# Performance work log

Measured on AMD Instinct MI355X. Metric: run time of the kernel, lower is better.

The kernel has to match this reference:

```python
import jax, jax.numpy as jnp
import numpy as np

D_MODEL = 1024
NUM_HEADS = 16
D_HEAD = D_MODEL // NUM_HEADS


def setup_inputs() -> dict:
    key = jax.random.key(0)
    kx, kq, kk, kv, ko = jax.random.split(key, 5)
    b, seq = 4, 2048
    x = jax.random.normal(kx, (b, seq, D_MODEL), dtype=jnp.float32)
    # Original uses ones for q/k/v and randn for output; use small random weights
    # for a numerically meaningful baseline of the same math.
    Wq = jax.random.normal(kq, (D_MODEL, D_MODEL), dtype=jnp.float32) * 0.02
    Wk = jax.random.normal(kk, (D_MODEL, D_MODEL), dtype=jnp.float32) * 0.02
    Wv = jax.random.normal(kv, (D_MODEL, D_MODEL), dtype=jnp.float32) * 0.02
    Wo = jax.random.normal(ko, (D_MODEL, D_MODEL), dtype=jnp.float32) * 0.02
    return {"x": x, "Wq": Wq, "Wk": Wk, "Wv": Wv, "Wo": Wo}


def reference(x, Wq, Wk, Wv, Wo):
    b, seq, d = x.shape
    h, dh = NUM_HEADS, D_HEAD

    def split_heads(t):  # [b, s, d] -> [b, h, s, dh]
        return t.reshape(b, seq, h, dh).transpose(0, 2, 1, 3)

    q = split_heads(x @ Wq.T)
    k = split_heads(x @ Wk.T)
    v = split_heads(x @ Wv.T)

    scores = jnp.einsum('bhqd,bhkd->bhqk', q, k) / jnp.sqrt(jnp.float32(dh))
    causal = jnp.tril(jnp.ones((seq, seq), dtype=bool))
    scores = jnp.where(causal, scores, -jnp.inf)
    attn = jax.nn.softmax(scores, axis=-1)
    out = jnp.einsum('bhqk,bhkd->bhqd', attn, v)  # [b, h, s, dh]
    out = out.transpose(0, 2, 1, 3).reshape(b, seq, d)
    return out @ Wo.T
```

## Files before the change

### kernel.cpp

```cpp
#include <hip/hip_runtime.h>
#include <stdint.h>

typedef unsigned short u16;
typedef __attribute__((ext_vector_type(8))) __bf16 bf16x8;
typedef __attribute__((ext_vector_type(4))) float f32x4;

#define AS1 __attribute__((address_space(1)))
#define AS3 __attribute__((address_space(3)))
#define LOG2E 1.4426950408889634f

__device__ __forceinline__ u16 f2bf(float f) {
    union { __bf16 h; u16 u; } cv;
    cv.h = (__bf16)f;
    return cv.u;
}

__device__ __forceinline__ float vmax4(f32x4 x) {
    return fmaxf(fmaxf(x[0], x[1]), fmaxf(x[2], x[3]));
}
__device__ __forceinline__ float vsum4(f32x4 x) {
    return (x[0] + x[1]) + (x[2] + x[3]);
}

__global__ __launch_bounds__(256) void cvt_kernel(
    const float* __restrict__ src, u16* __restrict__ dst, int n8)
{
    int i = blockIdx.x * 256 + threadIdx.x;
    if (i >= n8) return;
    const float4* s = (const float4*)src;
    float4 f0 = s[(size_t)i * 2], f1 = s[(size_t)i * 2 + 1];
    ushort4 a, b;
    a.x = f2bf(f0.x); a.y = f2bf(f0.y); a.z = f2bf(f0.z); a.w = f2bf(f0.w);
    b.x = f2bf(f1.x); b.y = f2bf(f1.y); b.z = f2bf(f1.z); b.w = f2bf(f1.w);
    ((ushort4*)dst)[(size_t)i * 2]     = a;
    ((ushort4*)dst)[(size_t)i * 2 + 1] = b;
}

__global__ __launch_bounds__(256) void cvt3_kernel(
    const float* __restrict__ wq, const float* __restrict__ wk,
    const float* __restrict__ wv, u16* __restrict__ dst)
{
    int i = blockIdx.x * 256 + threadIdx.x;
    int seg = i >> 17;
    const float* s = (seg == 0) ? wq : (seg == 1) ? wk : wv;
    float sc = (seg == 0) ? 0.125f : 1.0f;
    int j = i & 131071;
    const float4* sp = (const float4*)s;
    float4 f0 = sp[(size_t)j * 2], f1 = sp[(size_t)j * 2 + 1];
    ushort4 a, b;
    a.x = f2bf(f0.x * sc); a.y = f2bf(f0.y * sc); a.z = f2bf(f0.z * sc); a.w = f2bf(f0.w * sc);
    b.x = f2bf(f1.x * sc); b.y = f2bf(f1.y * sc); b.z = f2bf(f1.z * sc); b.w = f2bf(f1.w * sc);
    ((ushort4*)dst)[(size_t)i * 2]     = a;
    ((ushort4*)dst)[(size_t)i * 2 + 1] = b;
}

template <bool F32OUT>
__device__ __forceinline__ void gemm_tile_body(
    const u16* __restrict__ A, const u16* __restrict__ B, void* __restrict__ Cp,
    int K, int ldc, int mb, int nb, int cb, u16* As, u16* Bs)
{
    const int t  = threadIdx.x;
    const int l  = t & 63, w = t >> 6;
    const int wm = w >> 1, wn = w & 1;
    const int lr = l & 15, lg = l >> 4;

    f32x4 acc[4][4];
#pragma unroll
    for (int i = 0; i < 4; ++i)
#pragma unroll
        for (int j = 0; j < 4; ++j) acc[i][j] = f32x4{0.f, 0.f, 0.f, 0.f};

    for (int k0 = 0; k0 < K; k0 += 32) {
        __syncthreads();
#pragma unroll
        for (int i = 0; i < 2; ++i) {
            int chunk = i * 256 + t;
            int row   = chunk >> 2;
            int c8    = (chunk & 3) << 3;
            const u16* ga = A + (size_t)(mb + row) * K + k0 + c8;
            const u16* gb = B + (size_t)(nb + row) * K + k0 + c8;
            u16* la = As + (i * 256 + w * 64) * 8;
            u16* lb = Bs + (i * 256 + w * 64) * 8;
            __builtin_amdgcn_global_load_lds((AS1 unsigned int*)ga, (AS3 unsigned int*)la, 16, 0, 0);
            __builtin_amdgcn_global_load_lds((AS1 unsigned int*)gb, (AS3 unsigned int*)lb, 16, 0, 0);
        }
        __syncthreads();
        bf16x8 af[4], bfr[4];
#pragma unroll
        for (int mi = 0; mi < 4; ++mi)
            af[mi] = *(const bf16x8*)(As + (wm * 64 + mi * 16 + lr) * 32 + lg * 8);
#pragma unroll
        for (int ni = 0; ni < 4; ++ni)
            bfr[ni] = *(const bf16x8*)(Bs + (wn * 64 + ni * 16 + lr) * 32 + lg * 8);
#pragma unroll
        for (int mi = 0; mi < 4; ++mi)
#pragma unroll
            for (int ni = 0; ni < 4; ++ni)
                acc[mi][ni] = __builtin_amdgcn_mfma_f32_16x16x32_bf16(af[mi], bfr[ni], acc[mi][ni], 0, 0, 0);
    }
#pragma unroll
    for (int mi = 0; mi < 4; ++mi)
#pragma unroll
        for (int ni = 0; ni < 4; ++ni) {
            int col = cb + wn * 64 + ni * 16 + lr;
#pragma unroll
            for (int v = 0; v < 4; ++v) {
                int row = mb + wm * 64 + mi * 16 + lg * 4 + v;
                if (F32OUT)
                    ((float*)Cp)[(size_t)row * ldc + col] = acc[mi][ni][v];
                else
                    ((u16*)Cp)[(size_t)row * ldc + col] = f2bf(acc[mi][ni][v]);
            }
        }
}

__global__ __launch_bounds__(256, 2) void gemm_qkv_kernel(
    const u16* __restrict__ X, const u16* __restrict__ W3,
    u16* __restrict__ QKV)
{
    __shared__ __attribute__((aligned(16))) u16 As[128 * 32];
    __shared__ __attribute__((aligned(16))) u16 Bs[128 * 32];
    int bid = (int)blockIdx.x + (int)gridDim.x * (int)blockIdx.y;
    int wg  = (bid & 7) * 192 + (bid >> 3);
    int mx  = wg / 24;
    int my  = wg % 24;
    int wsel = my >> 3;
    const u16* B = W3 + (size_t)wsel * 1024 * 1024;
    int nb = (my & 7) * 128;
    gemm_tile_body<false>(X, B, QKV, 1024, 3072, mx * 128, nb, wsel * 1024 + nb, As, Bs);
}

__global__ __launch_bounds__(256, 2) void gemm_out_kernel(
    const u16* __restrict__ A, const u16* __restrict__ B, float* __restrict__ C)
{
    __shared__ __attribute__((aligned(16))) u16 As[128 * 32];
    __shared__ __attribute__((aligned(16))) u16 Bs[128 * 32];
    int bid = (int)blockIdx.x + (int)gridDim.x * (int)blockIdx.y;
    int wg  = (bid & 7) * 64 + (bid >> 3);
    int mx  = wg >> 3;
    int my  = wg & 7;
    gemm_tile_body<true>(A, B, C, 1024, 1024, mx * 128, my * 128, my * 128, As, Bs);
}

#define SEQ  2048
#define PSTR 72
#define NQT  16

__device__ __forceinline__ void attn_qtile(
    const u16* __restrict__ Qg, const u16* __restrict__ Kg, const u16* __restrict__ Vg,
    u16* __restrict__ outp, int b, int h, int qt,
    u16* QP, u16* Ks, u16* Vt)
{
    const int t  = threadIdx.x;
    const int l  = t & 63, w = t >> 6;
    const int lr = l & 15, lg = l >> 4;
    const int q0 = qt * 128;
    const int sr = t >> 3;
    const int sc = (t & 7) << 3;
    const int vswz = sc;

    __syncthreads();
#pragma unroll
    for (int i = 0; i < 4; ++i) {
        int r = sr + i * 32;
        *(uint4*)(QP + r * PSTR + sc) = *(const uint4*)(Qg + (size_t)(q0 + r) * 3072 + sc);
    }
    __syncthreads();
    bf16x8 qf[2][2];
#pragma unroll
    for (int mi = 0; mi < 2; ++mi)
#pragma unroll
        for (int ks = 0; ks < 2; ++ks)
            qf[mi][ks] = *(const bf16x8*)(QP + (w * 32 + mi * 16 + lr) * PSTR + ks * 32 + lg * 8);

    uint4 kpf[2], vpf[2];
#pragma unroll
    for (int i = 0; i < 2; ++i) {
        int r = sr + i * 32;
        kpf[i] = *(const uint4*)(Kg + (size_t)r * 3072 + sc);
        vpf[i] = *(const uint4*)(Vg + (size_t)r * 3072 + sc);
    }

    f32x4 o[4][2];
#pragma unroll
    for (int nd = 0; nd < 4; ++nd)
#pragma unroll
        for (int mi = 0; mi < 2; ++mi) o[nd][mi] = f32x4{0.f, 0.f, 0.f, 0.f};
    float mrow[2]  = { -__builtin_inff(), -__builtin_inff() };
    float mrowL[2] = { -__builtin_inff(), -__builtin_inff() };
    float lrow[2]  = { 0.f, 0.f };

    const int nkt = 2 * qt + 2;
    for (int kt = 0; kt < nkt; ++kt) {
        const int k0 = kt * 64;
        __syncthreads();
#pragma unroll
        for (int i = 0; i < 2; ++i) {
            int r = sr + i * 32;
            *(uint4*)(Ks + r * PSTR + sc) = kpf[i];
            int rs = r ^ vswz;
            union { uint4 q; u16 u[8]; } uv; uv.q = vpf[i];
#pragma unroll
            for (int j = 0; j < 8; ++j)
                Vt[(sc + j) * PSTR + rs] = uv.u[j];
        }
        if (kt + 1 < nkt) {
            const int k0n = k0 + 64;
#pragma unroll
            for (int i = 0; i < 2; ++i) {
                int r = sr + i * 32;
                kpf[i] = *(const uint4*)(Kg + (size_t)(k0n + r) * 3072 + sc);
                vpf[i] = *(const uint4*)(Vg + (size_t)(k0n + r) * 3072 + sc);
            }
        }
        __syncthreads();

        f32x4 s[4][2];
#pragma unroll
        for (int ni = 0; ni < 4; ++ni)
#pragma unroll
            for (int mi = 0; mi < 2; ++mi) s[ni][mi] = f32x4{0.f, 0.f, 0.f, 0.f};
        __builtin_amdgcn_s_setprio(1);
#pragma unroll
        for (int ks = 0; ks < 2; ++ks) {
            bf16x8 kb[4];
#pragma unroll
            for (int ni = 0; ni < 4; ++ni)
                kb[ni] = *(const bf16x8*)(Ks + (ni * 16 + lr) * PSTR + ks * 32 + lg * 8);
#pragma unroll
            for (int ni = 0; ni < 4; ++ni)
#pragma unroll
                for (int mi = 0; mi < 2; ++mi)
                    s[ni][mi] = __builtin_amdgcn_mfma_f32_16x16x32_bf16(kb[ni], qf[mi][ks], s[ni][mi], 0, 0, 0);
        }
        __builtin_amdgcn_s_setprio(0);

#pragma unroll
        for (int mi = 0; mi < 2; ++mi) {
            if ((k0 + 63) > (q0 + w * 32 + mi * 16)) {
                int qpos = q0 + w * 32 + mi * 16 + lr;
#pragma unroll
                for (int ni = 0; ni < 4; ++ni) {
                    int kb0 = k0 + ni * 16 + lg * 4;
#pragma unroll
                    for (int v = 0; v < 4; ++v)
                        if (kb0 + v > qpos) s[ni][mi][v] = -__builtin_inff();
                }
            }
        }

        float rmax[2];
        bool grew = false;
#pragma unroll
        for (int mi = 0; mi < 2; ++mi) {
            float r = fmaxf(fmaxf(vmax4(s[0][mi]), vmax4(s[1][mi])),
                            fmaxf(vmax4(s[2][mi]), vmax4(s[3][mi])));
            r = fmaxf(r, __shfl_xor(r, 16));
            r = fmaxf(r, __shfl_xor(r, 32));
            rmax[mi] = r;
            grew |= (r > mrow[mi]);
        }
        if (__ballot(grew)) {
#pragma unroll
            for (int mi = 0; mi < 2; ++mi) {
                float mn  = fmaxf(mrow[mi], rmax[mi]);
                float mnL = mn * LOG2E;
                float al  = __builtin_amdgcn_exp2f(mrowL[mi] - mnL);
                mrow[mi]  = mn;
                mrowL[mi] = mnL;
                lrow[mi] *= al;
#pragma unroll
                for (int nd = 0; nd < 4; ++nd)
#pragma unroll
                    for (int v = 0; v < 4; ++v) o[nd][mi][v] *= al;
            }
        }
#pragma unroll
        for (int mi = 0; mi < 2; ++mi) {
            float nmL = -mrowL[mi];
#pragma unroll
            for (int ni = 0; ni < 4; ++ni)
#pragma unroll
                for (int v = 0; v < 4; ++v)
                    s[ni][mi][v] = __builtin_amdgcn_exp2f(
                        __builtin_fmaf(s[ni][mi][v], LOG2E, nmL));
            float sum = (vsum4(s[0][mi]) + vsum4(s[1][mi]))
                      + (vsum4(s[2][mi]) + vsum4(s[3][mi]));
            sum += __shfl_xor(sum, 16);
            sum += __shfl_xor(sum, 32);
            lrow[mi] += sum;
            int prow = (w * 32 + mi * 16 + lr) * PSTR + lg * 4;
#pragma unroll
            for (int ni = 0; ni < 4; ++ni) {
                ushort4 u;
                u.x = f2bf(s[ni][mi][0]); u.y = f2bf(s[ni][mi][1]);
                u.z = f2bf(s[ni][mi][2]); u.w = f2bf(s[ni][mi][3]);
                *(ushort4*)(QP + prow + ni * 16) = u;
            }
        }

        __builtin_amdgcn_s_setprio(1);
#pragma unroll
        for (int ks = 0; ks < 2; ++ks) {
            bf16x8 pa[2], vb[4];
#pragma unroll
            for (int mi = 0; mi < 2; ++mi)
                pa[mi] = *(const bf16x8*)(QP + (w * 32 + mi * 16 + lr) * PSTR + ks * 32 + lg * 8);
#pragma unroll
            for (int nd = 0; nd < 4; ++nd) {
                int d = nd * 16 + lr;
                vb[nd] = *(const bf16x8*)(Vt + d * PSTR + ((ks * 32 + lg * 8) ^ (((d >> 3) & 7) << 3)));
            }
#pragma unroll
            for (int nd = 0; nd < 4; ++nd)
#pragma unroll
                for (int mi = 0; mi < 2; ++mi)
                    o[nd][mi] = __builtin_amdgcn_mfma_f32_16x16x32_bf16(vb[nd], pa[mi], o[nd][mi], 0, 0, 0);
        }
        __builtin_amdgcn_s_setprio(0);
    }

#pragma unroll
    for (int mi = 0; mi < 2; ++mi) {
        float inv = 1.f / lrow[mi];
        int row = q0 + w * 32 + mi * 16 + lr;
        u16* op = outp + (size_t)(b * SEQ + row) * 1024 + h * 64 + lg * 4;
#pragma unroll
        for (int nd = 0; nd < 4; ++nd) {
            ushort4 u;
            u.x = f2bf(o[nd][mi][0] * inv); u.y = f2bf(o[nd][mi][1] * inv);
            u.z = f2bf(o[nd][mi][2] * inv); u.w = f2bf(o[nd][mi][3] * inv);
            *(ushort4*)(op + nd * 16) = u;
        }
    }
}

__global__ __launch_bounds__(256, 2) void attn_kernel(
    const u16* __restrict__ qkv, u16* __restrict__ outp)
{
    __shared__ __attribute__((aligned(16))) u16 QP[128 * PSTR];
    __shared__ __attribute__((aligned(16))) u16 Ks[64 * PSTR];
    __shared__ __attribute__((aligned(16))) u16 Vt[64 * PSTR];

    const int bid = (int)blockIdx.x + (int)blockIdx.y * 8;
    const int xcd = bid & 7;
    const int j   = bid >> 3;
    const int bh  = xcd * 8 + (j & 7);
    const int qp  = j >> 3;
    const int b   = bh >> 4, h = bh & 15;

    const u16* Qg = qkv + (size_t)b * SEQ * 3072 + h * 64;
    const u16* Kg = Qg + 1024;
    const u16* Vg = Qg + 2048;

    attn_qtile(Qg, Kg, Vg, outp, b, h, qp,           QP, Ks, Vt);
    attn_qtile(Qg, Kg, Vg, outp, b, h, NQT - 1 - qp, QP, Ks, Vt);
}

extern "C" void kernel_launch(void* const* d_in, const int* in_sizes, int n_in,
                              void* d_out, int out_size, void* d_ws, size_t ws_size,
                              hipStream_t stream)
{
    (void)in_sizes; (void)n_in; (void)out_size; (void)ws_size;
    const float* x  = (const float*)d_in[0];
    const float* Wq = (const float*)d_in[1];
    const float* Wk = (const float*)d_in[2];
    const float* Wv = (const float*)d_in[3];
    const float* Wo = (const float*)d_in[4];

    u16*   qkv = (u16*)d_ws;
    u16*   xb  = qkv + (size_t)8192 * 3072;
    u16*   att = xb;
    u16*   w3  = (u16*)d_out;
    u16*   wob = qkv;
    float* out = (float*)d_out;

    cvt_kernel <<<dim3(4096), 256, 0, stream>>>(x, xb, 1048576);
    cvt3_kernel<<<dim3(1536), 256, 0, stream>>>(Wq, Wk, Wv, w3);

    gemm_qkv_kernel<<<dim3(64, 24), 256, 0, stream>>>(xb, w3, qkv);
    attn_kernel   <<<dim3(8, 64), 256, 0, stream>>>(qkv, att);

    cvt_kernel<<<dim3(512), 256, 0, stream>>>(Wo, wob, 131072);
    gemm_out_kernel<<<dim3(64, 8), 256, 0, stream>>>(att, wob, out);
}
```

Baseline: 275.7 us.

## Replace QKV GEMM with 256x256 tiled, double-buffered direct-to-LDS pipelined kernel

Replaces the 128x128 QKV projection GEMM with a 512-thread kernel that computes 256x256 output tiles. Operands are loaded with global_load_lds into a swizzled, double-buffered LDS layout using a K-step of 64. The K loop is split into four MFMA quadrants, with the next tile's loads interleaved between them, explicit vmcnt/lgkmcnt waits, barriers and setprio. The goal is to hide global-memory latency, raise arithmetic intensity and avoid LDS bank conflicts, at the cost of 128KB of LDS per block and heavier register pressure.

```diff
diff --git a/kernel.cpp b/kernel.cpp
--- a/kernel.cpp
+++ b/kernel.cpp
@@ -8,6 +8,12 @@
 #define AS1 __attribute__((address_space(1)))
 #define AS3 __attribute__((address_space(3)))
 #define LOG2E 1.4426950408889634f
+
+#define BAR() __builtin_amdgcn_s_barrier()
+#define LGKM0() do { asm volatile("s_waitcnt lgkmcnt(0)" ::: "memory"); \
+                     __builtin_amdgcn_sched_barrier(0); } while (0)
+#define VMC6() asm volatile("s_waitcnt vmcnt(6)" ::: "memory")
+#define VMC0() asm volatile("s_waitcnt vmcnt(0)" ::: "memory")
 
 __device__ __forceinline__ u16 f2bf(float f) {
     union { __bf16 h; u16 u; } cv;
@@ -54,10 +60,189 @@
     ((ushort4*)dst)[(size_t)i * 2 + 1] = b;
 }
 
-template <bool F32OUT>
-__device__ __forceinline__ void gemm_tile_body(
-    const u16* __restrict__ A, const u16* __restrict__ B, void* __restrict__ Cp,
-    int K, int ldc, int mb, int nb, int cb, u16* As, u16* Bs)
+#define LDS_OFF(p, h) ((((p) * 4 + (h)) * 8192))
+
+__device__ __forceinline__ void stage_A(
+    const u16* __restrict__ G, int kt, int hm, u16* region, int t)
+{
+    int w6 = t & ~63;
+#pragma unroll
+    for (int i = 0; i < 2; ++i) {
+        int s = i * 512 + t;
+        int r = s >> 3;
+        int j = (s & 7) ^ (r & 7);
+        int row = (r & 63) + ((r >> 6) << 7) + (hm << 6);
+        const u16* g = G + (size_t)row * 1024 + kt * 64 + j * 8;
+        u16* lp = region + (i * 512 + w6) * 8;
+        __builtin_amdgcn_global_load_lds((AS1 unsigned int*)g, (AS3 unsigned int*)lp, 16, 0, 0);
+    }
+}
+
+__device__ __forceinline__ void stage_B(
+    const u16* __restrict__ G, int kt, int hb, u16* region, int t)
+{
+    int w6 = t & ~63;
+#pragma unroll
+    for (int i = 0; i < 2; ++i) {
+        int s = i * 512 + t;
+        int r = s >> 3;
+        int j = (s & 7) ^ (r & 7);
+        int row = hb * 128 + r;
+        const u16* g = G + (size_t)row * 1024 + kt * 64 + j * 8;
+        u16* lp = region + (i * 512 + w6) * 8;
+        __builtin_amdgcn_global_load_lds((AS1 unsigned int*)g, (AS3 unsigned int*)lp, 16, 0, 0);
+    }
+}
+
+__device__ __forceinline__ bf16x8 fragr(const u16* region, int row, int j) {
+    int byte = row * 128 + ((j ^ (row & 7)) << 4);
+    return *(const bf16x8*)((const char*)region + byte);
+}
+
+__global__ __launch_bounds__(512, 2) void gemm_qkv_256(
+    const u16* __restrict__ X, const u16* __restrict__ W3, u16* __restrict__ QKV)
+{
+    __shared__ __attribute__((aligned(16))) u16 lds[65536];
+
+    const int t  = threadIdx.x;
+    const int l  = t & 63, w = t >> 6;
+    const int wm = w >> 2, wn = w & 3;
+    const int lr = l & 15, lg = l >> 4;
+
+    int bid = (int)blockIdx.x;
+    int wg  = (bid & 7) * 48 + (bid >> 3);
+    int mx  = wg / 12, ny = wg % 12;
+    const int mb = mx * 256, nb = ny * 256;
+    const u16* A = X  + (size_t)mb * 1024;
+    const u16* B = W3 + (size_t)nb * 1024;
+
+    const int NT = 16;
+
+    stage_A(A, 0, 0, lds + LDS_OFF(0, 0), t);
+    stage_B(B, 0, 0, lds + LDS_OFF(0, 2), t);
+    stage_B(B, 0, 1, lds + LDS_OFF(0, 3), t);
+    stage_A(A, 0, 1, lds + LDS_OFF(0, 1), t);
+    stage_A(A, 1, 0, lds + LDS_OFF(1, 0), t);
+    stage_B(B, 1, 0, lds + LDS_OFF(1, 2), t);
+    stage_B(B, 1, 1, lds + LDS_OFF(1, 3), t);
+    VMC6();
+    BAR();
+
+    f32x4 acc[8][4];
+#pragma unroll
+    for (int i = 0; i < 8; ++i)
+#pragma unroll
+        for (int j = 0; j < 4; ++j) acc[i][j] = f32x4{0.f, 0.f, 0.f, 0.f};
+
+    for (int kt = 0; kt < NT; ++kt) {
+        const int p = kt & 1;
+        u16* A0r = lds + LDS_OFF(p, 0);
+        u16* A1r = lds + LDS_OFF(p, 1);
+        u16* B0r = lds + LDS_OFF(p, 2);
+        u16* B1r = lds + LDS_OFF(p, 3);
+        u16* A1n = lds + LDS_OFF(p ^ 1, 1);
+        const u16* Bw = (wn >= 2) ? B1r : B0r;
+        const int brow0 = (wn & 1) * 64;
+
+        bf16x8 af[4][2], bf[4][2];
+
+#pragma unroll
+        for (int mi = 0; mi < 4; ++mi)
+#pragma unroll
+            for (int ks = 0; ks < 2; ++ks)
+                af[mi][ks] = fragr(A0r, wm * 64 + mi * 16 + lr, ks * 4 + lg);
+#pragma unroll
+        for (int ni = 0; ni < 2; ++ni)
+#pragma unroll
+            for (int ks = 0; ks < 2; ++ks)
+                bf[ni][ks] = fragr(Bw, brow0 + ni * 16 + lr, ks * 4 + lg);
+        if (kt + 1 < NT) stage_A(A, kt + 1, 1, A1n, t);
+        BAR();
+        LGKM0();
+        __builtin_amdgcn_s_setprio(1);
+#pragma unroll
+        for (int mi = 0; mi < 4; ++mi)
+#pragma unroll
+            for (int ni = 0; ni < 2; ++ni)
+#pragma unroll
+                for (int ks = 0; ks < 2; ++ks)
+                    acc[mi][ni] = __builtin_amdgcn_mfma_f32_16x16x32_bf16(af[mi][ks], bf[ni][ks], acc[mi][ni], 0, 0, 0);
+        __builtin_amdgcn_s_setprio(0);
+        BAR();
+
+#pragma unroll
+        for (int ni = 2; ni < 4; ++ni)
+#pragma unroll
+            for (int ks = 0; ks < 2; ++ks)
+                bf[ni][ks] = fragr(Bw, brow0 + ni * 16 + lr, ks * 4 + lg);
+        if (kt + 2 < NT) stage_A(A, kt + 2, 0, A0r, t);
+        BAR();
+        LGKM0();
+        __builtin_amdgcn_s_setprio(1);
+#pragma unroll
+        for (int mi = 0; mi < 4; ++mi)
+#pragma unroll
+            for (int ni = 2; ni < 4; ++ni)
+#pragma unroll
+                for (int ks = 0; ks < 2; ++ks)
+                    acc[mi][ni] = __builtin_amdgcn_mfma_f32_16x16x32_bf16(af[mi][ks], bf[ni][ks], acc[mi][ni], 0, 0, 0);
+        __builtin_amdgcn_s_setprio(0);
+        BAR();
+
+#pragma unroll
+        for (int mi = 0; mi < 4; ++mi)
+#pragma unroll
+            for (int ks = 0; ks < 2; ++ks)
+                af[mi][ks] = fragr(A1r, wm * 64 + mi * 16 + lr, ks * 4 + lg);
+        if (kt + 2 < NT) stage_B(B, kt + 2, 0, B0r, t);
+        BAR();
+        LGKM0();
+        __builtin_amdgcn_s_setprio(1);
+#pragma unroll
+        for (int mi = 0; mi < 4; ++mi)
+#pragma unroll
+            for (int ni = 0; ni < 2; ++ni)
+#pragma unroll
+                for (int ks = 0; ks < 2; ++ks)
+                    acc[4 + mi][ni] = __builtin_amdgcn_mfma_f32_16x16x32_bf16(af[mi][ks], bf[ni][ks], acc[4 + mi][ni], 0, 0, 0);
+        __builtin_amdgcn_s_setprio(0);
+        BAR();
+
+        if (kt + 2 < NT) {
+            stage_B(B, kt + 2, 1, B1r, t);
+            VMC6();
+        } else if (kt + 1 < NT) {
+            VMC0();
+        }
+        BAR();
+        __builtin_amdgcn_s_setprio(1);
+#pragma unroll
+        for (int mi = 0; mi < 4; ++mi)
+#pragma unroll
+            for (int ni = 2; ni < 4; ++ni)
+#pragma unroll
+                for (int ks = 0; ks < 2; ++ks)
+                    acc[4 + mi][ni] = __builtin_amdgcn_mfma_f32_16x16x32_bf16(af[mi][ks], bf[ni][ks], acc[4 + mi][ni], 0, 0, 0);
+        __builtin_amdgcn_s_setprio(0);
+        BAR();
+    }
+
+#pragma unroll
+    for (int mi = 0; mi < 8; ++mi)
+#pragma unroll
+        for (int ni = 0; ni < 4; ++ni) {
+            int col = nb + wn * 64 + ni * 16 + lr;
+#pragma unroll
+            for (int v = 0; v < 4; ++v) {
+                int row = mb + wm * 128 + mi * 16 + lg * 4 + v;
+                QKV[(size_t)row * 3072 + col] = f2bf(acc[mi][ni][v]);
+            }
+        }
+}
+
+__device__ __forceinline__ void gemm_tile_body_f32(
+    const u16* __restrict__ A, const u16* __restrict__ B, float* __restrict__ Cp,
+    int K, int ldc, int mb, int nb, u16* As, u16* Bs)
 {
     const int t  = threadIdx.x;
     const int l  = t & 63, w = t >> 6;
@@ -102,32 +287,13 @@
     for (int mi = 0; mi < 4; ++mi)
 #pragma unroll
         for (int ni = 0; ni < 4; ++ni) {
-            int col = cb + wn * 64 + ni * 16 + lr;
+            int col = nb + wn * 64 + ni * 16 + lr;
 #pragma unroll
             for (int v = 0; v < 4; ++v) {
                 int row = mb + wm * 64 + mi * 16 + lg * 4 + v;
-                if (F32OUT)
-                    ((float*)Cp)[(size_t)row * ldc + col] = acc[mi][ni][v];
-                else
-                    ((u16*)Cp)[(size_t)row * ldc + col] = f2bf(acc[mi][ni][v]);
-            }
-        }
-}
-
-__global__ __launch_bounds__(256, 2) void gemm_qkv_kernel(
-    const u16* __restrict__ X, const u16* __restrict__ W3,
-    u16* __restrict__ QKV)
-{
-    __shared__ __attribute__((aligned(16))) u16 As[128 * 32];
-    __shared__ __attribute__((aligned(16))) u16 Bs[128 * 32];
-    int bid = (int)blockIdx.x + (int)gridDim.x * (int)blockIdx.y;
-    int wg  = (bid & 7) * 192 + (bid >> 3);
-    int mx  = wg / 24;
-    int my  = wg % 24;
-    int wsel = my >> 3;
-    const u16* B = W3 + (size_t)wsel * 1024 * 1024;
-    int nb = (my & 7) * 128;
-    gemm_tile_body<false>(X, B, QKV, 1024, 3072, mx * 128, nb, wsel * 1024 + nb, As, Bs);
+                Cp[(size_t)row * ldc + col] = acc[mi][ni][v];
+            }
+        }
 }
 
 __global__ __launch_bounds__(256, 2) void gemm_out_kernel(
@@ -139,7 +305,7 @@
     int wg  = (bid & 7) * 64 + (bid >> 3);
     int mx  = wg >> 3;
     int my  = wg & 7;
-    gemm_tile_body<true>(A, B, C, 1024, 1024, mx * 128, my * 128, my * 128, As, Bs);
+    gemm_tile_body_f32(A, B, C, 1024, 1024, mx * 128, my * 128, As, Bs);
 }
 
 #define SEQ  2048
@@ -378,8 +544,8 @@
     cvt_kernel <<<dim3(4096), 256, 0, stream>>>(x, xb, 1048576);
     cvt3_kernel<<<dim3(1536), 256, 0, stream>>>(Wq, Wk, Wv, w3);
 
-    gemm_qkv_kernel<<<dim3(64, 24), 256, 0, stream>>>(xb, w3, qkv);
-    attn_kernel   <<<dim3(8, 64), 256, 0, stream>>>(qkv, att);
+    gemm_qkv_256<<<dim3(384), 512, 0, stream>>>(xb, w3, qkv);
+    attn_kernel <<<dim3(8, 64), 256, 0, stream>>>(qkv, att);
 
     cvt_kernel<<<dim3(512), 256, 0, stream>>>(Wo, wob, 131072);
     gemm_out_kernel<<<dim3(64, 8), 256, 0, stream>>>(att, wob, out);
```

Result: no change. 272.3 us (-1.2%).
